# Optimization experiments

Hardware: AMD Instinct MI355X
Metric: run time of the kernel (lower is better)

Reference implementation:

```python
import jax, jax.numpy as jnp
import numpy as np

EPS = 1e-5
N_HEADS = 8

def layer_norm(x, g, b):
    mu = x.mean(-1, keepdims=True)
    var = ((x - mu) ** 2).mean(-1, keepdims=True)
    return (x - mu) * jax.lax.rsqrt(var + EPS) * g + b

def rotate_half(x):
    d = x.shape[-1] // 2
    return jnp.concatenate([-x[..., d:], x[..., :d]], axis=-1)

def setup_inputs() -> dict:
    key = jax.random.key(0)
    ks = jax.random.split(key, 6)
    b, n, m, h, dh = 4, 512, 8192, N_HEADS, 16
    dim = h * dh
    s = dim ** -0.5
    return {
        "x": jax.random.normal(ks[0], (b, n, dim), jnp.float32),
        "mem_kv": jax.random.normal(ks[1], (b, h, m, 2 * dh), jnp.float32),
        "w_q": jax.random.normal(ks[2], (dim, dim), jnp.float32) * s,
        "w_kv": jax.random.normal(ks[3], (2 * dim, dim), jnp.float32) * s,
        "w_out": jax.random.normal(ks[4], (dim, dim), jnp.float32) * s,
        "b_out": jnp.zeros((dim,), jnp.float32),
        "g1": jnp.ones((dim,), jnp.float32),
        "b1": jnp.zeros((dim,), jnp.float32),
        "g2": jnp.ones((dim,), jnp.float32),
        "b2": jnp.zeros((dim,), jnp.float32),
    }

def reference(x, mem_kv, w_q, w_kv, w_out, b_out, g1, b1, g2, b2):
    b, n, dim = x.shape
    h = N_HEADS
    dh = dim // h
    # pre-norm + projections
    x_ = layer_norm(x, g1, b1)
    q = (x_ @ w_q.T).reshape(b, n, h, dh).transpose(0, 2, 1, 3)          # [b,h,n,dh]
    kv = (x_ @ w_kv.T).reshape(b, n, h, 2 * dh).transpose(0, 2, 1, 3)    # [b,h,n,2dh]
    mem_kv = jnp.concatenate([mem_kv, kv], axis=2)                        # growing cache
    k, v = jnp.split(mem_kv, 2, axis=-1)                                  # [b,h,j,dh] each
    q = q * dh ** -0.5
    # rotary embeddings (SinusoidalEmbeddings over k length, q uses trailing n positions)
    j = k.shape[2]
    inv_freq = 1.0 / (10000.0 ** (jnp.arange(0, dh, 2, dtype=jnp.float32) / dh))
    fr = jnp.arange(j, dtype=jnp.float32)[:, None] * inv_freq[None, :]
    freqs = jnp.concatenate([fr, fr], axis=-1)                            # [j, dh]
    cos, sin = jnp.cos(freqs), jnp.sin(freqs)
    q = q * cos[-n:] + rotate_half(q) * sin[-n:]
    k = k * cos + rotate_half(k) * sin
    # full attention of new chunk over cache (forward_simple, inference)
    sim = jnp.einsum('bhie,bhje->bhij', q, k)
    attn = jax.nn.softmax(sim, axis=-1)
    hv = jnp.einsum('bhij,bhje->bhie', attn, v)
    hv = hv.transpose(0, 2, 1, 3).reshape(b, n, dim) + x                  # residual
    out = layer_norm(hv, g2, b2) @ w_out.T + b_out + hv                   # out proj + residual
    return out, mem_kv
```

## Files before the change

### kernel.cpp

```cpp
#include <hip/hip_runtime.h>

#define B 4
#define N 512
#define M 8192
#define H 8
#define DH 16
#define DIM 128
#define J (M + N)
#define LN10000_DIV8 1.1512925465f
#define LOG2E 1.44269504f

typedef _Float16 f16;
typedef _Float16 half4 __attribute__((ext_vector_type(4)));
typedef _Float16 half8 __attribute__((ext_vector_type(8)));
typedef __fp16 fp16x2 __attribute__((ext_vector_type(2)));
typedef float f32x4 __attribute__((ext_vector_type(4)));

#if __has_builtin(__builtin_amdgcn_exp2f)
#define EXP2(x) __builtin_amdgcn_exp2f(x)
#else
#define EXP2(x) exp2f(x)
#endif

union PK { fp16x2 v; unsigned int u; };

__device__ __forceinline__ half8 pack8(float a, float b, float c, float d,
                                       float e, float f, float g, float h) {
#if __has_builtin(__builtin_amdgcn_cvt_pkrtz)
    union { unsigned int u[4]; half8 h8; } r;
    PK p0, p1, p2, p3;
    p0.v = __builtin_amdgcn_cvt_pkrtz(a, b);
    p1.v = __builtin_amdgcn_cvt_pkrtz(c, d);
    p2.v = __builtin_amdgcn_cvt_pkrtz(e, f);
    p3.v = __builtin_amdgcn_cvt_pkrtz(g, h);
    r.u[0] = p0.u; r.u[1] = p1.u; r.u[2] = p2.u; r.u[3] = p3.u;
    return r.h8;
#else
    half8 r = { (f16)a, (f16)b, (f16)c, (f16)d, (f16)e, (f16)f, (f16)g, (f16)h };
    return r;
#endif
}

#define WS_KROT 0ull
#define WS_VT   8912896ull
#define WS_QROT 17825792ull
#define WS_HV   18350080ull

union V4  { f16 h[4];  uint2 u; };

__device__ __forceinline__ half8 cvt8(const float* p) {
    float4 a = *(const float4*)p, b = *(const float4*)(p + 4);
    half8 h = { (f16)a.x, (f16)a.y, (f16)a.z, (f16)a.w,
                (f16)b.x, (f16)b.y, (f16)b.z, (f16)b.w };
    return h;
}

__global__ void __launch_bounds__(256) prep_proj_kernel(
    const f32x4* __restrict__ src, float4* __restrict__ dstv,
    f16* __restrict__ krot, f16* __restrict__ vt,
    const float* __restrict__ x, const float* __restrict__ g1,
    const float* __restrict__ b1, const float* __restrict__ wq,
    const float* __restrict__ wkv, f16* __restrict__ qrot)
{
    __shared__ __attribute__((aligned(16))) char smem[17408];

    if (blockIdx.x < 768) {
        f16 (*xnl)[136] = (f16 (*)[136])smem;
        float* out_mem = (float*)dstv;
        int w = threadIdx.x >> 6, lane = threadIdx.x & 63;
        int id = blockIdx.x * 4 + w;
        int ttile = id & 127, ctile = id >> 7;
        int token0 = ttile * 16;
        int col = lane & 15, quad = lane >> 4;

        {
            float g1a = g1[lane], g1b = g1[lane + 64];
            float b1a = b1[lane], b1b = b1[lane + 64];
            #pragma unroll 4
            for (int tt = 0; tt < 16; tt++) {
                int token = token0 + tt;
                float v0 = x[(size_t)token * DIM + lane];
                float v1 = x[(size_t)token * DIM + lane + 64];
                float s = v0 + v1;
                for (int off = 32; off; off >>= 1) s += __shfl_xor(s, off, 64);
                float mu = s * (1.0f / DIM);
                float d0 = v0 - mu, d1 = v1 - mu;
                float vs = d0 * d0 + d1 * d1;
                for (int off = 32; off; off >>= 1) vs += __shfl_xor(vs, off, 64);
                float rs = rsqrtf(vs * (1.0f / DIM) + 1e-5f);
                xnl[w * 16 + tt][lane]      = (f16)(d0 * rs * g1a + b1a);
                xnl[w * 16 + tt][lane + 64] = (f16)(d1 * rs * g1b + b1b);
            }
        }

        const float* wbase = (ctile < 8) ? (wq + (size_t)(ctile * 16 + col) * DIM)
                                         : (wkv + (size_t)((ctile - 8) * 16 + col) * DIM);
        const f16* arow = &xnl[w * 16 + col][quad * 8];

        f32x4 acc = {0.f, 0.f, 0.f, 0.f};
        #pragma unroll
        for (int kb = 0; kb < 4; kb++) {
            half8 a = *(const half8*)(arow + kb * 32);
            half8 wv = cvt8(wbase + kb * 32 + quad * 8);
            acc = __builtin_amdgcn_mfma_f32_16x16x32_f16(a, wv, acc, 0, 0, 0);
        }

        int e = col, r8 = e & 7;
        float f = __expf(-(float)r8 * LN10000_DIV8);
        int kt = ctile - 8;
        int head = (ctile < 8) ? ctile : (kt >> 1);
        int isV  = (ctile >= 8) ? (kt & 1) : 0;

        #pragma unroll
        for (int r = 0; r < 4; r++) {
            int tok = token0 + quad * 4 + r;
            int b = tok >> 9, i = tok & (N - 1);
            int bhh = b * H + head;
            float self = acc[r];
            float prt = __shfl_xor(self, 8, 64);

            if (ctile < 8) {
                float ang = (float)(M + i) * f;
                float sn, cs; __sincosf(ang, &sn, &cs);
                float rv = (self * cs + ((e < 8) ? -prt : prt) * sn) * (0.25f * LOG2E);
                qrot[((size_t)bhh * N + i) * 16 + e] = (f16)rv;
            } else if (!isV) {
                out_mem[((size_t)bhh * J + M + i) * 32 + e] = self;
                float ang = (float)(M + i) * f;
                float sn, cs; __sincosf(ang, &sn, &cs);
                float rv = self * cs + ((e < 8) ? -prt : prt) * sn;
                int jpos = M + i;
                int tilei = jpos >> 5, jj = jpos & 31;
                int col4 = (jj >> 3) * 4 + (jj & 3), frag = (jj >> 2) & 1;
                krot[(size_t)bhh * J * 16 + (size_t)tilei * 512 +
                     (e >> 2) * 128 + col4 * 8 + frag * 4 + (e & 3)] = (f16)rv;
            } else {
                out_mem[((size_t)bhh * J + M + i) * 32 + 16 + e] = self;
                vt[(size_t)bhh * 16 * J + (size_t)e * J + M + i] = (f16)self;
            }
        }
    } else {
        float (*tile)[33] = (float (*)[33])smem;
        int bid = blockIdx.x - 768;
        int bh = bid >> 7;
        int j0 = (bid & 127) * 64;
        int t = threadIdx.x;

        #pragma unroll
        for (int rep = 0; rep < 2; rep++) {
            int idx = t + rep * 256;
            int row = idx >> 3, c4 = idx & 7;
            f32x4 v = __builtin_nontemporal_load(src + ((size_t)bh * M + j0 + row) * 8 + c4);
            __builtin_nontemporal_store(v,
                (f32x4*)dstv + ((size_t)bh * J + j0 + row) * 8 + c4);
            tile[row][c4 * 4 + 0] = v[0]; tile[row][c4 * 4 + 1] = v[1];
            tile[row][c4 * 4 + 2] = v[2]; tile[row][c4 * 4 + 3] = v[3];
        }
        __syncthreads();

        if (t < 128) {
            int row = t >> 1, rh = t & 1;
            int j = j0 + row;
            float lo4[4], hi4[4];
            #pragma unroll
            for (int i = 0; i < 4; i++) {
                int r = rh * 4 + i;
                float ang = (float)j * __expf(-(float)r * LN10000_DIV8);
                float sn, cs; __sincosf(ang, &sn, &cs);
                float lo = tile[row][r], hi = tile[row][r + 8];
                lo4[i] = lo * cs - hi * sn;
                hi4[i] = hi * cs + lo * sn;
            }
            int tilei = j >> 5, jj = j & 31;
            int col4 = (jj >> 3) * 4 + (jj & 3), frag = (jj >> 2) & 1;
            f16* base = krot + (size_t)bh * J * 16 + (size_t)tilei * 512 + col4 * 8 + frag * 4;
            V4 wl, wh;
            #pragma unroll
            for (int i = 0; i < 4; i++) { wl.h[i] = (f16)lo4[i]; wh.h[i] = (f16)hi4[i]; }
            *(uint2*)(base + rh * 128)       = wl.u;
            *(uint2*)(base + (2 + rh) * 128) = wh.u;
        }
        {
            int dh = t >> 4, c0 = (t & 15) * 4;
            V4 vv;
            #pragma unroll
            for (int i = 0; i < 4; i++) vv.h[i] = (f16)tile[c0 + i][16 + dh];
            *(uint2*)(vt + (size_t)bh * 16 * J + (size_t)dh * J + j0 + c0) = vv.u;
        }
    }
}

__global__ void __launch_bounds__(1024) attn_kernel(
    const f16* __restrict__ krot, const f16* __restrict__ vt,
    const f16* __restrict__ qrot, f16* __restrict__ hvw)
{
    __shared__ float sacc[16][2][256];
    __shared__ float sl[16][2][16];
    int bh = blockIdx.x & 31;
    int q0 = (blockIdx.x >> 5) * 32;
    int wave = threadIdx.x >> 6, lane = threadIdx.x & 63;
    int col = lane & 15, quad = lane >> 4;

    const f16* vb = vt + (size_t)bh * 16 * J + (size_t)col * J;
    half4 qfa = *(const half4*)(qrot + ((size_t)bh * N + q0 + col) * 16 + quad * 4);
    half4 qfb = *(const half4*)(qrot + ((size_t)bh * N + q0 + 16 + col) * 16 + quad * 4);

    int jstart = wave * (J / 16);
    const f16* kptr = krot + (size_t)bh * J * 16 + (size_t)jstart * 16 + lane * 8;
    const f16* vptr = vb + jstart + quad * 8;

    f32x4 acca = {0.f, 0.f, 0.f, 0.f};
    f32x4 accb = {0.f, 0.f, 0.f, 0.f};
    f32x4 accla = {0.f, 0.f, 0.f, 0.f};
    f32x4 acclb = {0.f, 0.f, 0.f, 0.f};
    const f32x4 zero = {0.f, 0.f, 0.f, 0.f};
    const half8 ones = { (f16)1.f, (f16)1.f, (f16)1.f, (f16)1.f,
                         (f16)1.f, (f16)1.f, (f16)1.f, (f16)1.f };

    #pragma unroll 2
    for (int it = 0; it < 17; ++it) {
        half8 kf8 = *(const half8*)kptr;
        half8 vf  = *(const half8*)vptr;
        kptr += 512; vptr += 32;
        half4 kf0 = __builtin_shufflevector(kf8, kf8, 0, 1, 2, 3);
        half4 kf1 = __builtin_shufflevector(kf8, kf8, 4, 5, 6, 7);
        __builtin_amdgcn_s_setprio(1);
        f32x4 s0a = __builtin_amdgcn_mfma_f32_16x16x16f16(kf0, qfa, zero, 0, 0, 0);
        f32x4 s1a = __builtin_amdgcn_mfma_f32_16x16x16f16(kf1, qfa, zero, 0, 0, 0);
        f32x4 s0b = __builtin_amdgcn_mfma_f32_16x16x16f16(kf0, qfb, zero, 0, 0, 0);
        f32x4 s1b = __builtin_amdgcn_mfma_f32_16x16x16f16(kf1, qfb, zero, 0, 0, 0);
        __builtin_amdgcn_s_setprio(0);

        float a0 = EXP2(s0a[0]), a1 = EXP2(s0a[1]), a2 = EXP2(s0a[2]), a3 = EXP2(s0a[3]);
        float a4 = EXP2(s1a[0]), a5 = EXP2(s1a[1]), a6 = EXP2(s1a[2]), a7 = EXP2(s1a[3]);
        float b0 = EXP2(s0b[0]), b1 = EXP2(s0b[1]), b2 = EXP2(s0b[2]), b3 = EXP2(s0b[3]);
        float b4 = EXP2(s1b[0]), b5 = EXP2(s1b[1]), b6 = EXP2(s1b[2]), b7 = EXP2(s1b[3]);
        half8 pfa = pack8(a0, a1, a2, a3, a4, a5, a6, a7);
        half8 pfb = pack8(b0, b1, b2, b3, b4, b5, b6, b7);
        __builtin_amdgcn_s_setprio(1);
        acca  = __builtin_amdgcn_mfma_f32_16x16x32_f16(pfa, vf,   acca,  0, 0, 0);
        accla = __builtin_amdgcn_mfma_f32_16x16x32_f16(pfa, ones, accla, 0, 0, 0);
        accb  = __builtin_amdgcn_mfma_f32_16x16x32_f16(pfb, vf,   accb,  0, 0, 0);
        acclb = __builtin_amdgcn_mfma_f32_16x16x32_f16(pfb, ones, acclb, 0, 0, 0);
        __builtin_amdgcn_s_setprio(0);
    }

    if (col == 0) {
        #pragma unroll
        for (int r = 0; r < 4; r++) {
            sl[wave][0][quad * 4 + r] = accla[r];
            sl[wave][1][quad * 4 + r] = acclb[r];
        }
    }
    #pragma unroll
    for (int r = 0; r < 4; r++) {
        sacc[wave][0][(quad * 4 + r) * 16 + col] = acca[r];
        sacc[wave][1][(quad * 4 + r) * 16 + col] = accb[r];
    }
    __syncthreads();

    if (threadIdx.x < 512) {
        int t = threadIdx.x;
        int qt = t >> 8, ql = (t >> 4) & 15, c = t & 15;
        float o = 0.f, lt = 0.f;
        #pragma unroll
        for (int w = 0; w < 16; w++) {
            o  += sacc[w][qt][ql * 16 + c];
            lt += sl[w][qt][ql];
        }
        int b = bh >> 3, h = bh & 7;
        hvw[((size_t)(b * N) + q0 + qt * 16 + ql) * DIM + h * DH + c] = (f16)(o / lt);
    }
}

__global__ void __launch_bounds__(256) final_kernel(
    const f16* __restrict__ hvw, const float* __restrict__ x,
    const float* __restrict__ wout, const float* __restrict__ bout,
    const float* __restrict__ g2, const float* __restrict__ b2v,
    float* __restrict__ out)
{
    __shared__ f16 xn2[16][136];
    __shared__ float hres[16][132];
    int token0 = (blockIdx.x >> 1) * 16;
    int half = blockIdx.x & 1;
    int wave = threadIdx.x >> 6, lane = threadIdx.x & 63;

    #pragma unroll
    for (int tt = 0; tt < 4; tt++) {
        int tl = wave * 4 + tt;
        int token = token0 + tl;
        float h0 = (float)hvw[(size_t)token * DIM + lane]      + x[(size_t)token * DIM + lane];
        float h1 = (float)hvw[(size_t)token * DIM + lane + 64] + x[(size_t)token * DIM + lane + 64];
        float s = h0 + h1;
        for (int off = 32; off; off >>= 1) s += __shfl_xor(s, off, 64);
        float mu = s * (1.0f / DIM);
        float d0 = h0 - mu, d1 = h1 - mu;
        float vs = d0 * d0 + d1 * d1;
        for (int off = 32; off; off >>= 1) vs += __shfl_xor(vs, off, 64);
        float rs = rsqrtf(vs * (1.0f / DIM) + 1e-5f);
        xn2[tl][lane]      = (f16)(d0 * rs * g2[lane]      + b2v[lane]);
        xn2[tl][lane + 64] = (f16)(d1 * rs * g2[lane + 64] + b2v[lane + 64]);
        hres[tl][lane] = h0; hres[tl][lane + 64] = h1;
    }
    __syncthreads();

    int col = lane & 15, quad = lane >> 4;
    int ct = half * 4 + wave;
    int cg = ct * 16 + col;
    const float* wrow = wout + (size_t)cg * DIM;
    f32x4 acc = {0.f, 0.f, 0.f, 0.f};
    #pragma unroll
    for (int kb = 0; kb < 4; kb++) {
        half8 a = *(const half8*)(&xn2[col][kb * 32 + quad * 8]);
        half8 w = cvt8(wrow + kb * 32 + quad * 8);
        acc = __builtin_amdgcn_mfma_f32_16x16x32_f16(a, w, acc, 0, 0, 0);
    }
    float bo = bout[cg];
    #pragma unroll
    for (int r = 0; r < 4; r++) {
        int tl = quad * 4 + r;
        out[(size_t)(token0 + tl) * DIM + cg] = acc[r] + bo + hres[tl][cg];
    }
}

extern "C" void kernel_launch(void* const* d_in, const int* in_sizes, int n_in,
                              void* d_out, int out_size, void* d_ws, size_t ws_size,
                              hipStream_t stream)
{
    const float* x      = (const float*)d_in[0];
    const float* mem_kv = (const float*)d_in[1];
    const float* wq     = (const float*)d_in[2];
    const float* wkv    = (const float*)d_in[3];
    const float* wout   = (const float*)d_in[4];
    const float* bout   = (const float*)d_in[5];
    const float* g1     = (const float*)d_in[6];
    const float* b1     = (const float*)d_in[7];
    const float* g2     = (const float*)d_in[8];
    const float* b2     = (const float*)d_in[9];

    float* out = (float*)d_out;
    float* out_mem = out + (size_t)B * N * DIM;

    f16* krot = (f16*)((char*)d_ws + WS_KROT);
    f16* vt   = (f16*)((char*)d_ws + WS_VT);
    f16* qrot = (f16*)((char*)d_ws + WS_QROT);
    f16* hvw  = (f16*)((char*)d_ws + WS_HV);

    hipLaunchKernelGGL(prep_proj_kernel, dim3(4864), dim3(256), 0, stream,
                       (const f32x4*)mem_kv, (float4*)out_mem, krot, vt,
                       x, g1, b1, wq, wkv, qrot);
    hipLaunchKernelGGL(attn_kernel, dim3(512), dim3(1024), 0, stream,
                       krot, vt, qrot, hvw);
    hipLaunchKernelGGL(final_kernel, dim3(256), dim3(256), 0, stream,
                       hvw, x, wout, bout, g2, b2, out);
}
```

Before: 139.9 us.

## Process 64 queries per attention block with 8 waves to reuse K/V loads

The attention kernel now assigns 64 query rows per block (four 16-row tiles) instead of 32, with 8 waves each scanning twice as many keys. Every K/V fragment loaded is reused across four query tiles instead of two, halving K/V global traffic per query. The grid shrinks from 512 to 256 blocks of 512 threads, and the setprio hints and unroll pragma are dropped. Register pressure rises with eight accumulators, and fewer blocks may reduce occupancy or latency hiding.

```diff
diff --git a/kernel.cpp b/kernel.cpp
--- a/kernel.cpp
+++ b/kernel.cpp
@@ -190,86 +190,91 @@
     }
 }
 
-__global__ void __launch_bounds__(1024) attn_kernel(
+__global__ void __launch_bounds__(512, 2) attn_kernel(
     const f16* __restrict__ krot, const f16* __restrict__ vt,
     const f16* __restrict__ qrot, f16* __restrict__ hvw)
 {
-    __shared__ float sacc[16][2][256];
-    __shared__ float sl[16][2][16];
+    __shared__ float sacc[8][4][256];
+    __shared__ float sl[8][4][16];
     int bh = blockIdx.x & 31;
-    int q0 = (blockIdx.x >> 5) * 32;
+    int q0 = (blockIdx.x >> 5) * 64;
     int wave = threadIdx.x >> 6, lane = threadIdx.x & 63;
     int col = lane & 15, quad = lane >> 4;
 
     const f16* vb = vt + (size_t)bh * 16 * J + (size_t)col * J;
-    half4 qfa = *(const half4*)(qrot + ((size_t)bh * N + q0 + col) * 16 + quad * 4);
-    half4 qfb = *(const half4*)(qrot + ((size_t)bh * N + q0 + 16 + col) * 16 + quad * 4);
-
-    int jstart = wave * (J / 16);
+    const f16* qb = qrot + ((size_t)bh * N + q0 + col) * 16 + quad * 4;
+    half4 qf0 = *(const half4*)(qb);
+    half4 qf1 = *(const half4*)(qb + 16 * 16);
+    half4 qf2 = *(const half4*)(qb + 32 * 16);
+    half4 qf3 = *(const half4*)(qb + 48 * 16);
+
+    int jstart = wave * (J / 8);
     const f16* kptr = krot + (size_t)bh * J * 16 + (size_t)jstart * 16 + lane * 8;
     const f16* vptr = vb + jstart + quad * 8;
 
-    f32x4 acca = {0.f, 0.f, 0.f, 0.f};
-    f32x4 accb = {0.f, 0.f, 0.f, 0.f};
-    f32x4 accla = {0.f, 0.f, 0.f, 0.f};
-    f32x4 acclb = {0.f, 0.f, 0.f, 0.f};
+    f32x4 acc0 = {0.f,0.f,0.f,0.f}, acc1 = {0.f,0.f,0.f,0.f};
+    f32x4 acc2 = {0.f,0.f,0.f,0.f}, acc3 = {0.f,0.f,0.f,0.f};
+    f32x4 accl0 = {0.f,0.f,0.f,0.f}, accl1 = {0.f,0.f,0.f,0.f};
+    f32x4 accl2 = {0.f,0.f,0.f,0.f}, accl3 = {0.f,0.f,0.f,0.f};
     const f32x4 zero = {0.f, 0.f, 0.f, 0.f};
     const half8 ones = { (f16)1.f, (f16)1.f, (f16)1.f, (f16)1.f,
                          (f16)1.f, (f16)1.f, (f16)1.f, (f16)1.f };
 
-    #pragma unroll 2
-    for (int it = 0; it < 17; ++it) {
+    for (int it = 0; it < 34; ++it) {
         half8 kf8 = *(const half8*)kptr;
         half8 vf  = *(const half8*)vptr;
         kptr += 512; vptr += 32;
         half4 kf0 = __builtin_shufflevector(kf8, kf8, 0, 1, 2, 3);
         half4 kf1 = __builtin_shufflevector(kf8, kf8, 4, 5, 6, 7);
-        __builtin_amdgcn_s_setprio(1);
-        f32x4 s0a = __builtin_amdgcn_mfma_f32_16x16x16f16(kf0, qfa, zero, 0, 0, 0);
-        f32x4 s1a = __builtin_amdgcn_mfma_f32_16x16x16f16(kf1, qfa, zero, 0, 0, 0);
-        f32x4 s0b = __builtin_amdgcn_mfma_f32_16x16x16f16(kf0, qfb, zero, 0, 0, 0);
-        f32x4 s1b = __builtin_amdgcn_mfma_f32_16x16x16f16(kf1, qfb, zero, 0, 0, 0);
-        __builtin_amdgcn_s_setprio(0);
-
-        float a0 = EXP2(s0a[0]), a1 = EXP2(s0a[1]), a2 = EXP2(s0a[2]), a3 = EXP2(s0a[3]);
-        float a4 = EXP2(s1a[0]), a5 = EXP2(s1a[1]), a6 = EXP2(s1a[2]), a7 = EXP2(s1a[3]);
-        float b0 = EXP2(s0b[0]), b1 = EXP2(s0b[1]), b2 = EXP2(s0b[2]), b3 = EXP2(s0b[3]);
-        float b4 = EXP2(s1b[0]), b5 = EXP2(s1b[1]), b6 = EXP2(s1b[2]), b7 = EXP2(s1b[3]);
-        half8 pfa = pack8(a0, a1, a2, a3, a4, a5, a6, a7);
-        half8 pfb = pack8(b0, b1, b2, b3, b4, b5, b6, b7);
-        __builtin_amdgcn_s_setprio(1);
-        acca  = __builtin_amdgcn_mfma_f32_16x16x32_f16(pfa, vf,   acca,  0, 0, 0);
-        accla = __builtin_amdgcn_mfma_f32_16x16x32_f16(pfa, ones, accla, 0, 0, 0);
-        accb  = __builtin_amdgcn_mfma_f32_16x16x32_f16(pfb, vf,   accb,  0, 0, 0);
-        acclb = __builtin_amdgcn_mfma_f32_16x16x32_f16(pfb, ones, acclb, 0, 0, 0);
-        __builtin_amdgcn_s_setprio(0);
+
+#define QTILE(QF, ACC, ACCL)                                                     \
+        {                                                                        \
+            f32x4 s0 = __builtin_amdgcn_mfma_f32_16x16x16f16(kf0, QF, zero, 0, 0, 0); \
+            f32x4 s1 = __builtin_amdgcn_mfma_f32_16x16x16f16(kf1, QF, zero, 0, 0, 0); \
+            float e0 = EXP2(s0[0]), e1 = EXP2(s0[1]), e2 = EXP2(s0[2]), e3 = EXP2(s0[3]); \
+            float e4 = EXP2(s1[0]), e5 = EXP2(s1[1]), e6 = EXP2(s1[2]), e7 = EXP2(s1[3]); \
+            half8 pf = pack8(e0, e1, e2, e3, e4, e5, e6, e7);                    \
+            ACC  = __builtin_amdgcn_mfma_f32_16x16x32_f16(pf, vf,   ACC,  0, 0, 0); \
+            ACCL = __builtin_amdgcn_mfma_f32_16x16x32_f16(pf, ones, ACCL, 0, 0, 0); \
+        }
+        QTILE(qf0, acc0, accl0)
+        QTILE(qf1, acc1, accl1)
+        QTILE(qf2, acc2, accl2)
+        QTILE(qf3, acc3, accl3)
+#undef QTILE
     }
 
     if (col == 0) {
         #pragma unroll
         for (int r = 0; r < 4; r++) {
-            sl[wave][0][quad * 4 + r] = accla[r];
-            sl[wave][1][quad * 4 + r] = acclb[r];
+            sl[wave][0][quad * 4 + r] = accl0[r];
+            sl[wave][1][quad * 4 + r] = accl1[r];
+            sl[wave][2][quad * 4 + r] = accl2[r];
+            sl[wave][3][quad * 4 + r] = accl3[r];
         }
     }
     #pragma unroll
     for (int r = 0; r < 4; r++) {
-        sacc[wave][0][(quad * 4 + r) * 16 + col] = acca[r];
-        sacc[wave][1][(quad * 4 + r) * 16 + col] = accb[r];
+        sacc[wave][0][(quad * 4 + r) * 16 + col] = acc0[r];
+        sacc[wave][1][(quad * 4 + r) * 16 + col] = acc1[r];
+        sacc[wave][2][(quad * 4 + r) * 16 + col] = acc2[r];
+        sacc[wave][3][(quad * 4 + r) * 16 + col] = acc3[r];
     }
     __syncthreads();
 
-    if (threadIdx.x < 512) {
-        int t = threadIdx.x;
-        int qt = t >> 8, ql = (t >> 4) & 15, c = t & 15;
-        float o = 0.f, lt = 0.f;
-        #pragma unroll
-        for (int w = 0; w < 16; w++) {
-            o  += sacc[w][qt][ql * 16 + c];
-            lt += sl[w][qt][ql];
-        }
+    {
         int b = bh >> 3, h = bh & 7;
-        hvw[((size_t)(b * N) + q0 + qt * 16 + ql) * DIM + h * DH + c] = (f16)(o / lt);
+        #pragma unroll
+        for (int o = threadIdx.x; o < 1024; o += 512) {
+            int qt = o >> 8, ql = (o >> 4) & 15, c = o & 15;
+            float os = 0.f, lt = 0.f;
+            #pragma unroll
+            for (int w = 0; w < 8; w++) {
+                os += sacc[w][qt][ql * 16 + c];
+                lt += sl[w][qt][ql];
+            }
+            hvw[((size_t)(b * N) + q0 + qt * 16 + ql) * DIM + h * DH + c] = (f16)(os / lt);
+        }
     }
 }
 
@@ -349,7 +354,7 @@
     hipLaunchKernelGGL(prep_proj_kernel, dim3(4864), dim3(256), 0, stream,
                        (const f32x4*)mem_kv, (float4*)out_mem, krot, vt,
                        x, g1, b1, wq, wkv, qrot);
-    hipLaunchKernelGGL(attn_kernel, dim3(512), dim3(1024), 0, stream,
+    hipLaunchKernelGGL(attn_kernel, dim3(256), dim3(512), 0, stream,
                        krot, vt, qrot, hvw);
     hipLaunchKernelGGL(final_kernel, dim3(256), dim3(256), 0, stream,
                        hvw, x, wout, bout, g2, b2, out);
```

Measured after the change: 146.8 us. +4.9%, slower.
